# Optimization experiments

Measured on AMD Instinct MI355X. Metric: run time of the kernel, lower is better.

Reference implementation:

```python
import jax, jax.numpy as jnp
import numpy as np

N_ATOMS = 50000
N_EDGES = 600000
N_FEAT = 128      # n_atom_basis
N_FILT = 128      # n_filters
N_GAUSS = 32
N_CONV = 3
CUTOFF = 5.0
ATOMS_PER_MOL = 50
N_MOL = N_ATOMS // ATOMS_PER_MOL
N_KEYS = 2        # energy_0, energy_1
HIDDEN_RO = 64
LOG2 = float(np.log(2.0))


def ssp(x):
    # shifted softplus: softplus(x) - log(2)
    return jax.nn.softplus(x) - LOG2


def setup_inputs() -> dict:
    key = jax.random.key(0)
    ks = jax.random.split(key, 16)
    def w(k, shape, fan_in):
        return jax.random.normal(k, shape, dtype=jnp.float32) / np.sqrt(fan_in)
    return {
        "z": jax.random.randint(ks[0], (N_ATOMS,), 1, 100),
        "xyz": jax.random.normal(ks[1], (N_ATOMS, 3), dtype=jnp.float32) * 4.0,
        "nbr_list": jax.random.randint(ks[2], (N_EDGES, 2), 0, N_ATOMS),
        "mol_idx": jnp.arange(N_ATOMS, dtype=jnp.int32) // ATOMS_PER_MOL,
        "embed": jax.random.normal(ks[3], (100, N_FEAT), dtype=jnp.float32) * 0.1,
        "We1": w(ks[4], (N_CONV, N_GAUSS, N_FILT), N_GAUSS),
        "be1": jnp.zeros((N_CONV, N_FILT), jnp.float32),
        "We2": w(ks[5], (N_CONV, N_FILT, N_FILT), N_FILT),
        "be2": jnp.zeros((N_CONV, N_FILT), jnp.float32),
        "Wn": w(ks[6], (N_CONV, N_FEAT, N_FILT), N_FEAT),
        "bn": jnp.zeros((N_CONV, N_FILT), jnp.float32),
        "Wu1": w(ks[7], (N_CONV, N_FILT, N_FEAT), N_FILT),
        "bu1": jnp.zeros((N_CONV, N_FEAT), jnp.float32),
        "Wu2": w(ks[8], (N_CONV, N_FEAT, N_FEAT), N_FEAT),
        "bu2": jnp.zeros((N_CONV, N_FEAT), jnp.float32),
        "Wr1": w(ks[9], (N_KEYS, N_FEAT, HIDDEN_RO), N_FEAT),
        "br1": jnp.zeros((N_KEYS, HIDDEN_RO), jnp.float32),
        "Wr2": w(ks[10], (N_KEYS, HIDDEN_RO, 1), HIDDEN_RO),
        "br2": jnp.zeros((N_KEYS, 1), jnp.float32),
    }


def _forward(xyz, embed, We1, be1, We2, be2, Wn, bn, Wu1, bu1, Wu2, bu2,
             Wr1, br1, Wr2, br2, z, nbr_list, mol_idx):
    a0, a1 = nbr_list[:, 0], nbr_list[:, 1]
    # pairwise distances e = ||xyz_i - xyz_j||  -> [E,1]
    diff = xyz[a0] - xyz[a1]
    d = jnp.sqrt(jnp.sum(diff * diff, axis=1, keepdims=True))
    # Gaussian smearing on [0, cutoff]
    offs = jnp.linspace(0.0, CUTOFF, N_GAUSS).astype(xyz.dtype)
    width = offs[1] - offs[0]
    gauss = jnp.exp((-0.5 / (width * width)) * (d - offs[None, :]) ** 2)  # [E,G]
    r = embed[z]  # [N,F] atom embedding lookup
    for l in range(N_CONV):
        # edge filter MLP: G -> Filt -> Filt
        ef = ssp(gauss @ We1[l] + be1[l]) @ We2[l] + be2[l]       # [E,Filt]
        rf = r @ Wn[l] + bn[l]                                    # [N,Filt]
        m_ij = rf[a0] * ef                                        # gather * filter
        m_ji = rf[a1] * ef
        agg = (jax.ops.segment_sum(m_ij, a1, num_segments=N_ATOMS)
               + jax.ops.segment_sum(m_ji, a0, num_segments=N_ATOMS))
        # update MLP, residual add
        r = r + (ssp(agg @ Wu1[l] + bu1[l]) @ Wu2[l] + bu2[l])
    # per-key atomwise readout: F -> H -> 1
    h = ssp(jnp.einsum('nf,kfh->knh', r, Wr1) + br1[:, None, :])          # [K,N,H]
    e_atom = (jnp.einsum('knh,kho->kno', h, Wr2) + br2[:, None, :])[..., 0]  # [K,N]
    # sum atom energies per molecule (batch_and_sum)
    e_mol = jax.ops.segment_sum(e_atom.T, mol_idx, num_segments=N_MOL)    # [M,K]
    return e_mol


def reference(z, xyz, nbr_list, mol_idx, embed, We1, be1, We2, be2, Wn, bn,
              Wu1, bu1, Wu2, bu2, Wr1, br1, Wr2, br2):
    return _forward(xyz, embed, We1, be1, We2, be2, Wn, bn, Wu1, bu1,
                    Wu2, bu2, Wr1, br1, Wr2, br2, z, nbr_list, mol_idx)
```

## Files before the change

kernel.cpp:

```cpp
#include <hip/hip_runtime.h>
#include <math.h>

#define N_ATOMS   50000
#define N_PAD     50048
#define N_EDGES   600000
#define N_FEAT    128
#define N_GAUSS   32
#define N_CONV    3
#define N_MOLS    1000
#define HIDDEN_RO 64
#define CAP       64

#define TBL_N     1921
#define TBL_BPL   31
#define TBL_SCALE 256.0f
#define TBL_TMAX  1919.0f
#define NB_EDGE   2344
#define NB_BUILD  (N_CONV * TBL_BPL)
#define NB_EMBG   7
#define NB_WPREP  40

typedef unsigned int   uint32;
typedef unsigned short u16;
typedef __attribute__((ext_vector_type(8))) short bf16x8;
typedef __attribute__((ext_vector_type(4))) float f32x4;

__device__ __forceinline__ float ssp_f(float x) {
    float e = __expf(-fabsf(x));
    return fmaxf(x, 0.0f) + __logf(1.0f + e) - 0.6931471805599453f;
}
__device__ __forceinline__ uint32 f2bf_u(float x) {
    uint32 u = __float_as_uint(x);
    return (u + 0x7fffu + ((u >> 16) & 1u)) >> 16;
}
__device__ __forceinline__ uint32 pack2f(float a, float b) {
    return f2bf_u(a) | (f2bf_u(b) << 16);
}
__device__ __forceinline__ float bf_lo(uint32 u) { return __uint_as_float(u << 16); }
__device__ __forceinline__ float bf_hi(uint32 u) { return __uint_as_float(u & 0xffff0000u); }


#define FILL_START (NB_BUILD + NB_EMBG + NB_WPREP)
__global__ __launch_bounds__(256)
void k_uberA(const int* __restrict__ nbr, const float* __restrict__ xyz,
             int* __restrict__ cnt, uint32* __restrict__ inc32,
             const float* __restrict__ We1_all, const float* __restrict__ be1_all,
             const float* __restrict__ We2_all, const float* __restrict__ be2_all,
             uint32* __restrict__ tblI,
             const float* __restrict__ Wn, const float* __restrict__ bn,
             const float* __restrict__ Wu1,
             const float* __restrict__ Wu2, const float* __restrict__ Wr1,
             u16* __restrict__ Wt, const float* __restrict__ embed,
             float* __restrict__ Gp) {
    __shared__ float smemA[17408 / 4];
    int b = blockIdx.x;
    int t = threadIdx.x;

    if (b < NB_BUILD) {
        int l    = b / TBL_BPL;
        int row0 = (b % TBL_BPL) * 64;
        const float* We1 = We1_all + (size_t)l * N_GAUSS * N_FEAT;
        const float* be1 = be1_all + (size_t)l * N_FEAT;
        const float* We2 = We2_all + (size_t)l * N_FEAT * N_FEAT;
        const float* be2 = be2_all + (size_t)l * N_FEAT;
        uint32* tl = tblI + (size_t)l * TBL_N * 128;
        u16* h1T = (u16*)smemA;

        const float width = 5.0f / 31.0f;
        const float coef = -0.5f / (width * width);

        int tf = t & 15, te = t >> 4;
        int f0 = tf * 8, eb = te * 4;
        float dloc[4];
        #pragma unroll
        for (int i = 0; i < 4; ++i) dloc[i] = (float)(row0 + eb + i) * (1.0f / TBL_SCALE);

        float acc[4][8];
        #pragma unroll
        for (int i = 0; i < 4; ++i)
            #pragma unroll
            for (int j = 0; j < 8; ++j) acc[i][j] = 0.0f;

        for (int g = 0; g < N_GAUSS; ++g) {
            float mu = (float)g * width;
            float av[4];
            #pragma unroll
            for (int i = 0; i < 4; ++i) {
                float diff = dloc[i] - mu;
                av[i] = __expf(coef * diff * diff);
            }
            float4 w0 = *(const float4*)(We1 + g * N_FEAT + f0);
            float4 w1 = *(const float4*)(We1 + g * N_FEAT + f0 + 4);
            float wv[8] = {w0.x, w0.y, w0.z, w0.w, w1.x, w1.y, w1.z, w1.w};
            #pragma unroll
            for (int i = 0; i < 4; ++i)
                #pragma unroll
                for (int j = 0; j < 8; ++j) acc[i][j] += av[i] * wv[j];
        }
        #pragma unroll
        for (int j = 0; j < 8; ++j) {
            float bb2 = be1[f0 + j];
            uint2 hv;
            hv.x = pack2f(ssp_f(acc[0][j] + bb2), ssp_f(acc[1][j] + bb2));
            hv.y = pack2f(ssp_f(acc[2][j] + bb2), ssp_f(acc[3][j] + bb2));
            *(uint2*)&h1T[(f0 + j) * 68 + eb] = hv;
        }
        __syncthreads();

        #pragma unroll
        for (int i = 0; i < 4; ++i)
            #pragma unroll
            for (int j = 0; j < 8; ++j) acc[i][j] = 0.0f;
        #pragma unroll 2
        for (int c = 0; c < N_FEAT; ++c) {
            uint2 hv = *(const uint2*)&h1T[c * 68 + eb];
            float av[4] = {bf_lo(hv.x), bf_hi(hv.x), bf_lo(hv.y), bf_hi(hv.y)};
            float4 w0 = *(const float4*)(We2 + c * N_FEAT + f0);
            float4 w1 = *(const float4*)(We2 + c * N_FEAT + f0 + 4);
            float wv[8] = {w0.x, w0.y, w0.z, w0.w, w1.x, w1.y, w1.z, w1.w};
            #pragma unroll
            for (int i = 0; i < 4; ++i)
                #pragma unroll
                for (int j = 0; j < 8; ++j) acc[i][j] += av[i] * wv[j];
        }
        __syncthreads();

        uint32* pvS = (uint32*)smemA;
        #pragma unroll
        for (int i = 0; i < 4; ++i)
            #pragma unroll
            for (int p = 0; p < 4; ++p)
                pvS[(eb + i) * 65 + tf * 4 + p] =
                    pack2f(acc[i][2 * p]     + be2[f0 + 2 * p],
                           acc[i][2 * p + 1] + be2[f0 + 2 * p + 1]);
        __syncthreads();

        #pragma unroll
        for (int i = 0; i < 16; ++i) {
            int idx = t + 256 * i;
            int e = idx >> 6, fp = idx & 63;
            int ent = row0 + e;
            if (ent < TBL_N - 1) {
                if (e < 63) {
                    uint2 v2;
                    v2.x = pvS[e * 65 + fp];
                    v2.y = pvS[(e + 1) * 65 + fp];
                    *(uint2*)(tl + ((size_t)ent * 64 + fp) * 2) = v2;
                } else {
                    tl[((size_t)ent * 64 + fp) * 2] = pvS[63 * 65 + fp];
                }
            }
        }
        if (row0 > 0 && t < 64)
            tl[((size_t)(row0 - 1) * 64 + t) * 2 + 1] = pvS[t];
        return;
    }
    if (b < NB_BUILD + NB_EMBG) {
        int bb = b - NB_BUILD;
        int row = bb * 16 + (t >> 4);
        int tf = t & 15;
        if (row < 100) {
            float acc[8];
            #pragma unroll
            for (int j = 0; j < 8; ++j) acc[j] = 0.0f;
            for (int k = 0; k < N_FEAT; ++k) {
                float a = embed[row * N_FEAT + k];
                float4 w0 = *(const float4*)(Wn + k * N_FEAT + tf * 8);
                float4 w1 = *(const float4*)(Wn + k * N_FEAT + tf * 8 + 4);
                acc[0] += a * w0.x; acc[1] += a * w0.y;
                acc[2] += a * w0.z; acc[3] += a * w0.w;
                acc[4] += a * w1.x; acc[5] += a * w1.y;
                acc[6] += a * w1.z; acc[7] += a * w1.w;
            }
            #pragma unroll
            for (int j = 0; j < 8; ++j)
                Gp[row * N_FEAT + tf * 8 + j] = acc[j] + bn[tf * 8 + j];
        }
        return;
    }
    if (b < FILL_START) {
        int wb = b - NB_BUILD - NB_EMBG;
        int gid = wb * 256 + t;
        #pragma unroll
        for (int i = 0; i < 16; ++i) {
            int idx = gid + i * (NB_WPREP * 256);
            int j    = idx & 7;
            int lane = (idx >> 3) & 63;
            int cg   = (idx >> 9) & 7;
            int kc   = (idx >> 12) & 3;
            int mat  = idx >> 14;
            int col  = cg * 16 + (lane & 15);
            int k    = kc * 32 + (lane >> 4) * 8 + j;
            float v;
            if (mat < 3)      v = Wn [(size_t)mat * 16384 + k * 128 + col];
            else if (mat < 6) v = Wu1[(size_t)(mat - 3) * 16384 + k * 128 + col];
            else if (mat < 9) v = Wu2[(size_t)(mat - 6) * 16384 + k * 128 + col];
            else { int key = col >> 6, h = col & 63; v = Wr1[(size_t)key * 128 * 64 + k * 64 + h]; }
            Wt[(size_t)idx] = (u16)f2bf_u(v);
        }
        return;
    }
    {
        int cls = b & 7;
        int base = ((b - FILL_START) >> 3) * 2048;
        #pragma unroll
        for (int i = 0; i < 8; ++i) {
            int e = base + t + 256 * i;
            if (e < N_EDGES) {
                int a0 = nbr[2 * e], a1 = nbr[2 * e + 1];
                bool m0 = (a0 & 7) == cls, m1 = (a1 & 7) == cls;
                if (m0 | m1) {
                    float dx = xyz[3 * a0]     - xyz[3 * a1];
                    float dy = xyz[3 * a0 + 1] - xyz[3 * a1 + 1];
                    float dz = xyz[3 * a0 + 2] - xyz[3 * a1 + 2];
                    float d = sqrtf(dx * dx + dy * dy + dz * dz);
                    float tv = fminf(d * TBL_SCALE, TBL_TMAX);
                    uint32 tq = (uint32)(tv * 32.0f + 0.5f);
                    if (m1) {
                        int p1 = atomicAdd(&cnt[a1], 1);
                        if (p1 < CAP) inc32[((size_t)a1 << 6) | p1] = ((uint32)a0 << 16) | tq;
                    }
                    if (m0) {
                        int p0 = atomicAdd(&cnt[a0], 1);
                        if (p0 < CAP) inc32[((size_t)a0 << 6) | p0] = ((uint32)a1 << 16) | tq;
                    }
                }
            }
        }
    }
}

__global__ __launch_bounds__(256)
void k_gather(const int* __restrict__ z, const float* __restrict__ embed,
              const float* __restrict__ Gp, float* __restrict__ r,
              uint32* __restrict__ rf16) {
    int idx = blockIdx.x * 256 + threadIdx.x;
    if (idx >= N_PAD * 32) return;
    int n = idx >> 5, c4 = idx & 31;
    int zz = z[n < N_ATOMS ? n : 0];
    float4 v = *(const float4*)(embed + (size_t)zz * N_FEAT + c4 * 4);
    *(float4*)(r + (size_t)n * N_FEAT + c4 * 4) = v;
    float4 g = *(const float4*)(Gp + (size_t)zz * N_FEAT + c4 * 4);
    uint2 o;
    o.x = pack2f(g.x, g.y);
    o.y = pack2f(g.z, g.w);
    *(uint2*)(rf16 + (size_t)n * 64 + c4 * 2) = o;
}

__global__ __launch_bounds__(256)
void k_agg(const int* __restrict__ cnt, const uint32* __restrict__ inc32,
           const uint32* __restrict__ tblI, const uint32* __restrict__ rf,
           uint32* __restrict__ agg16) {
    int wv = threadIdx.x >> 6, lane = threadIdx.x & 63;
    int h = lane >> 5, lh = lane & 31;
    int n = blockIdx.x * 4 + wv;
    if (n >= N_ATOMS) return;
    int s = n << 6;
    int e = s + min(cnt[n], CAP);
    float a0 = 0.f, a1 = 0.f, a2 = 0.f, a3 = 0.f;
    int i = s;
    for (; i + 8 <= e; i += 8) {
        uint32 v[4];
        #pragma unroll
        for (int u = 0; u < 4; ++u) v[u] = inc32[i + 2 * u + h];
        int i0[4], oa[4];
        float fr[4];
        #pragma unroll
        for (int u = 0; u < 4; ++u) {
            oa[u] = v[u] >> 16;
            uint32 tq = v[u] & 0xffffu;
            i0[u] = tq >> 5;
            fr[u] = (float)(tq & 31u) * 0.03125f;
        }
        uint4 T[4];
        #pragma unroll
        for (int u = 0; u < 4; ++u) T[u] = *(const uint4*)(tblI + ((size_t)i0[u] * 64 + lh * 2) * 2);
        uint2 R[4];
        #pragma unroll
        for (int u = 0; u < 4; ++u) R[u] = *(const uint2*)(rf + (size_t)oa[u] * 64 + lh * 2);
        #pragma unroll
        for (int u = 0; u < 4; ++u) {
            float e0 = fmaf(fr[u], bf_lo(T[u].y) - bf_lo(T[u].x), bf_lo(T[u].x));
            float e1 = fmaf(fr[u], bf_hi(T[u].y) - bf_hi(T[u].x), bf_hi(T[u].x));
            float e2 = fmaf(fr[u], bf_lo(T[u].w) - bf_lo(T[u].z), bf_lo(T[u].z));
            float e3 = fmaf(fr[u], bf_hi(T[u].w) - bf_hi(T[u].z), bf_hi(T[u].z));
            a0 = fmaf(e0, bf_lo(R[u].x), a0);
            a1 = fmaf(e1, bf_hi(R[u].x), a1);
            a2 = fmaf(e2, bf_lo(R[u].y), a2);
            a3 = fmaf(e3, bf_hi(R[u].y), a3);
        }
    }
    for (; i < e; i += 2) {
        int idx = i + h;
        bool ok = idx < e;
        uint32 v = inc32[ok ? idx : s];
        int oa = v >> 16;
        uint32 tq = v & 0xffffu;
        int i0 = tq >> 5;
        float fr = (float)(tq & 31u) * 0.03125f;
        uint4 T = *(const uint4*)(tblI + ((size_t)i0 * 64 + lh * 2) * 2);
        uint2 R = *(const uint2*)(rf + (size_t)oa * 64 + lh * 2);
        float m = ok ? 1.0f : 0.0f;
        float e0 = fmaf(fr, bf_lo(T.y) - bf_lo(T.x), bf_lo(T.x));
        float e1 = fmaf(fr, bf_hi(T.y) - bf_hi(T.x), bf_hi(T.x));
        float e2 = fmaf(fr, bf_lo(T.w) - bf_lo(T.z), bf_lo(T.z));
        float e3 = fmaf(fr, bf_hi(T.w) - bf_hi(T.z), bf_hi(T.z));
        a0 = fmaf(e0, m * bf_lo(R.x), a0);
        a1 = fmaf(e1, m * bf_hi(R.x), a1);
        a2 = fmaf(e2, m * bf_lo(R.y), a2);
        a3 = fmaf(e3, m * bf_hi(R.y), a3);
    }
    a0 += __shfl_xor(a0, 32);
    a1 += __shfl_xor(a1, 32);
    a2 += __shfl_xor(a2, 32);
    a3 += __shfl_xor(a3, 32);
    if (h == 0) {
        uint2 o;
        o.x = pack2f(a0, a1);
        o.y = pack2f(a2, a3);
        *(uint2*)(agg16 + (size_t)n * 64 + lh * 2) = o;
    }
}

template <bool RO>
__global__ __launch_bounds__(256)
void k_update(const u16* __restrict__ agg16u,
              const float* __restrict__ bu1, const float* __restrict__ bu2,
              const u16* __restrict__ Wu1t, const u16* __restrict__ Wu2t,
              const u16* __restrict__ W3t, const float* __restrict__ b3,
              float* __restrict__ r, u16* __restrict__ rf16,
              const float* __restrict__ Wr2, const float* __restrict__ br2,
              const int* __restrict__ mol, float* __restrict__ out) {
    __shared__ u16 aT[32 * 136];
    __shared__ u16 hT[32 * 136];

    int tid = threadIdx.x;
    int w = tid >> 6, lane = tid & 63;
    int l15 = lane & 15, q = lane >> 4;
    int colbase = w * 32;
    size_t n0 = (size_t)blockIdx.x * 32;
    size_t fragoff = (size_t)(w * 2) * 512 + (size_t)lane * 8;

    bf16x8 bfr[4][2];
    #pragma unroll
    for (int kc = 0; kc < 4; ++kc)
        #pragma unroll
        for (int ntl = 0; ntl < 2; ++ntl)
            bfr[kc][ntl] = *(const bf16x8*)(Wu1t + kc * 4096 + ntl * 512 + fragoff);
    float rpre[2][2][4];
    #pragma unroll
    for (int ntl = 0; ntl < 2; ++ntl) {
        int col = colbase + ntl * 16 + l15;
        #pragma unroll
        for (int m = 0; m < 2; ++m)
            #pragma unroll
            for (int reg = 0; reg < 4; ++reg)
                rpre[ntl][m][reg] = r[(n0 + m * 16 + q * 4 + reg) * N_FEAT + col];
    }

    #pragma unroll
    for (int i = 0; i < 2; ++i) {
        int idx = tid + 256 * i;
        int row = idx >> 4, c = idx & 15;
        uint4 v = *(const uint4*)(agg16u + (n0 + row) * 128 + c * 8);
        *(uint4*)&aT[row * 136 + c * 8] = v;
    }
    __syncthreads();

    f32x4 acc[2][2];

    #pragma unroll
    for (int m = 0; m < 2; ++m)
        #pragma unroll
        for (int ntl = 0; ntl < 2; ++ntl) acc[m][ntl] = (f32x4){0.f, 0.f, 0.f, 0.f};
    #pragma unroll
    for (int kc = 0; kc < 4; ++kc)
        #pragma unroll
        for (int m = 0; m < 2; ++m) {
            bf16x8 a = *(const bf16x8*)(aT + (m * 16 + l15) * 136 + kc * 32 + q * 8);
            acc[m][0] = __builtin_amdgcn_mfma_f32_16x16x32_bf16(a, bfr[kc][0], acc[m][0], 0, 0, 0);
            acc[m][1] = __builtin_amdgcn_mfma_f32_16x16x32_bf16(a, bfr[kc][1], acc[m][1], 0, 0, 0);
        }
    #pragma unroll
    for (int ntl = 0; ntl < 2; ++ntl) {
        int col = colbase + ntl * 16 + l15;
        float bv = bu1[col];
        #pragma unroll
        for (int m = 0; m < 2; ++m)
            #pragma unroll
            for (int reg = 0; reg < 4; ++reg)
                hT[(m * 16 + q * 4 + reg) * 136 + col] = (u16)f2bf_u(ssp_f(acc[m][ntl][reg] + bv));
    }
    __syncthreads();

    #pragma unroll
    for (int kc = 0; kc < 4; ++kc)
        #pragma unroll
        for (int ntl = 0; ntl < 2; ++ntl)
            bfr[kc][ntl] = *(const bf16x8*)(Wu2t + kc * 4096 + ntl * 512 + fragoff);
    #pragma unroll
    for (int m = 0; m < 2; ++m)
        #pragma unroll
        for (int ntl = 0; ntl < 2; ++ntl) acc[m][ntl] = (f32x4){0.f, 0.f, 0.f, 0.f};
    #pragma unroll
    for (int kc = 0; kc < 4; ++kc)
        #pragma unroll
        for (int m = 0; m < 2; ++m) {
            bf16x8 a = *(const bf16x8*)(hT + (m * 16 + l15) * 136 + kc * 32 + q * 8);
            acc[m][0] = __builtin_amdgcn_mfma_f32_16x16x32_bf16(a, bfr[kc][0], acc[m][0], 0, 0, 0);
            acc[m][1] = __builtin_amdgcn_mfma_f32_16x16x32_bf16(a, bfr[kc][1], acc[m][1], 0, 0, 0);
        }
    __syncthreads();
    #pragma unroll
    for (int ntl = 0; ntl < 2; ++ntl) {
        int col = colbase + ntl * 16 + l15;
        float bv = bu2[col];
        #pragma unroll
        for (int m = 0; m < 2; ++m)
            #pragma unroll
            for (int reg = 0; reg < 4; ++reg) {
                int row = m * 16 + q * 4 + reg;
                float v = acc[m][ntl][reg] + bv + rpre[ntl][m][reg];
                if (!RO) r[(n0 + row) * N_FEAT + col] = v;
                aT[row * 136 + col] = (u16)f2bf_u(v);
            }
    }
    __syncthreads();

    #pragma unroll
    for (int kc = 0; kc < 4; ++kc)
        #pragma unroll
        for (int ntl = 0; ntl < 2; ++ntl)
            bfr[kc][ntl] = *(const bf16x8*)(W3t + kc * 4096 + ntl * 512 + fragoff);
    #pragma unroll
    for (int m = 0; m < 2; ++m)
        #pragma unroll
        for (int ntl = 0; ntl < 2; ++ntl) acc[m][ntl] = (f32x4){0.f, 0.f, 0.f, 0.f};
    #pragma unroll
    for (int kc = 0; kc < 4; ++kc)
        #pragma unroll
        for (int m = 0; m < 2; ++m) {
            bf16x8 a = *(const bf16x8*)(aT + (m * 16 + l15) * 136 + kc * 32 + q * 8);
            acc[m][0] = __builtin_amdgcn_mfma_f32_16x16x32_bf16(a, bfr[kc][0], acc[m][0], 0, 0, 0);
            acc[m][1] = __builtin_amdgcn_mfma_f32_16x16x32_bf16(a, bfr[kc][1], acc[m][1], 0, 0, 0);
        }

    if (!RO) {
        #pragma unroll
        for (int ntl = 0; ntl < 2; ++ntl) {
            int col = colbase + ntl * 16 + l15;
            float bv = b3[col];
            #pragma unroll
            for (int m = 0; m < 2; ++m)
                #pragma unroll
                for (int reg = 0; reg < 4; ++reg) {
                    int row = m * 16 + q * 4 + reg;
                    rf16[(n0 + row) * N_FEAT + col] = (u16)f2bf_u(acc[m][ntl][reg] + bv);
                }
        }
    } else {
        float (*red)[4][17] = (float(*)[4][17])aT;
        __syncthreads();
        float b1v[2], w2v[2];
        #pragma unroll
        for (int ntl = 0; ntl < 2; ++ntl) {
            int col = colbase + ntl * 16 + l15;
            b1v[ntl] = b3[col];
            w2v[ntl] = Wr2[col];
        }
        #pragma unroll
        for (int m = 0; m < 2; ++m)
            #pragma unroll
            for (int reg = 0; reg < 4; ++reg) {
                float pk = ssp_f(acc[m][0][reg] + b1v[0]) * w2v[0]
                         + ssp_f(acc[m][1][reg] + b1v[1]) * w2v[1];
                red[m * 16 + q * 4 + reg][w][l15] = pk;
            }
        __syncthreads();
        if (tid < 64) {
            int row = tid & 31, key = tid >> 5;
            int atom = (int)n0 + row;
            if (atom < N_ATOMS) {
                float s = br2[key];
                #pragma unroll
                for (int j = 0; j < 16; ++j)
                    s += red[row][2 * key][j] + red[row][2 * key + 1][j];
                atomicAdd(&out[mol[atom] * 2 + key], s);
            }
        }
    }
}

extern "C" void kernel_launch(void* const* d_in, const int* in_sizes, int n_in,
                              void* d_out, int out_size, void* d_ws, size_t ws_size,
                              hipStream_t stream) {
    const int*   z     = (const int*)d_in[0];
    const float* xyz   = (const float*)d_in[1];
    const int*   nbr   = (const int*)d_in[2];
    const int*   mol   = (const int*)d_in[3];
    const float* embed = (const float*)d_in[4];
    const float* We1   = (const float*)d_in[5];
    const float* be1   = (const float*)d_in[6];
    const float* We2   = (const float*)d_in[7];
    const float* be2   = (const float*)d_in[8];
    const float* Wn    = (const float*)d_in[9];
    const float* bn    = (const float*)d_in[10];
    const float* Wu1   = (const float*)d_in[11];
    const float* bu1   = (const float*)d_in[12];
    const float* Wu2   = (const float*)d_in[13];
    const float* bu2   = (const float*)d_in[14];
    const float* Wr1   = (const float*)d_in[15];
    const float* br1   = (const float*)d_in[16];
    const float* Wr2   = (const float*)d_in[17];
    const float* br2   = (const float*)d_in[18];
    float* out = (float*)d_out;

    float* ws = (float*)d_ws;
    const size_t NRP = (size_t)N_PAD * N_FEAT;
    const size_t NHP = (size_t)N_PAD * 64;
    float*  r_buf  = ws;
    uint32* agg16  = (uint32*)(ws + NRP);
    uint32* rf16   = agg16 + NHP;
    int*    cnt    = (int*)(rf16 + NHP);
    uint32* inc32  = (uint32*)(cnt + 50048);
    uint32* tblI   = inc32 + (size_t)N_ATOMS * CAP;
    u16*    Wt     = (u16*)(tblI + (size_t)3 * TBL_N * 128);
    float*  Gp     = (float*)(Wt + 10 * 16384);

    hipMemsetAsync(d_out, 0, (size_t)out_size * sizeof(float), stream);
    hipMemsetAsync(cnt, 0, 50000 * sizeof(int), stream);

    k_uberA<<<FILL_START + NB_EDGE, 256, 0, stream>>>(
        nbr, xyz, cnt, inc32, We1, be1, We2, be2, tblI,
        Wn, bn, Wu1, Wu2, Wr1, Wt, embed, Gp);

    k_gather<<<(N_PAD * 32) / 256, 256, 0, stream>>>(z, embed, Gp, r_buf, rf16);

    const int GA2 = N_PAD / 32;
    for (int l = 0; l < N_CONV; ++l) {
        k_agg<<<(N_ATOMS + 3) / 4, 256, 0, stream>>>(cnt, inc32,
                                                     tblI + (size_t)l * TBL_N * 128,
                                                     rf16, agg16);
        const u16* Wu1t = Wt + (size_t)(3 + l) * 16384;
        const u16* Wu2t = Wt + (size_t)(6 + l) * 16384;
        if (l < N_CONV - 1) {
            k_update<false><<<GA2, 256, 0, stream>>>((const u16*)agg16, bu1 + l * 128,
                                                     bu2 + l * 128, Wu1t, Wu2t,
                                                     Wt + (size_t)(l + 1) * 16384,
                                                     bn + (l + 1) * 128,
                                                     r_buf, (u16*)rf16, Wr2, br2, mol, out);
        } else {
            k_update<true><<<GA2, 256, 0, stream>>>((const u16*)agg16, bu1 + l * 128,
                                                    bu2 + l * 128, Wu1t, Wu2t,
                                                    Wt + (size_t)9 * 16384, br1,
                                                    r_buf, (u16*)rf16, Wr2, br2, mol, out);
        }
    }
}
```

Baseline: 412.3 us.

## Merge memsets and embed GEMV into pre-kernel, fold gather into uber kernel

Replaces the two hipMemsetAsync calls with a small pre-kernel that also computes the embedding-times-Wn table, then folds the atom gather into the big uber kernel. Edge-fill blocks now come first so the long edge scatter starts early. In k_agg, each wave loads its 64 incidence entries once and broadcasts them with shuffles instead of reloading per step. The aim is fewer launches and less redundant global loading, at the cost of one extra dependency stage for the precomputed table.

Result: no change. 406.4 us, median of 3 (-1.4%).

```diff
diff --git a/kernel.cpp b/kernel.cpp
--- a/kernel.cpp
+++ b/kernel.cpp
@@ -17,8 +17,11 @@
 #define TBL_TMAX  1919.0f
 #define NB_EDGE   2344
 #define NB_BUILD  (N_CONV * TBL_BPL)
-#define NB_EMBG   7
 #define NB_WPREP  40
+#define NB_GATH   6256
+#define BUILD_START NB_EDGE
+#define WPREP_START (NB_EDGE + NB_BUILD)
+#define GATH_START  (NB_EDGE + NB_BUILD + NB_WPREP)
 
 typedef unsigned int   uint32;
 typedef unsigned short u16;
@@ -39,125 +42,13 @@
 __device__ __forceinline__ float bf_lo(uint32 u) { return __uint_as_float(u << 16); }
 __device__ __forceinline__ float bf_hi(uint32 u) { return __uint_as_float(u & 0xffff0000u); }
 
-
-#define FILL_START (NB_BUILD + NB_EMBG + NB_WPREP)
 __global__ __launch_bounds__(256)
-void k_uberA(const int* __restrict__ nbr, const float* __restrict__ xyz,
-             int* __restrict__ cnt, uint32* __restrict__ inc32,
-             const float* __restrict__ We1_all, const float* __restrict__ be1_all,
-             const float* __restrict__ We2_all, const float* __restrict__ be2_all,
-             uint32* __restrict__ tblI,
-             const float* __restrict__ Wn, const float* __restrict__ bn,
-             const float* __restrict__ Wu1,
-             const float* __restrict__ Wu2, const float* __restrict__ Wr1,
-             u16* __restrict__ Wt, const float* __restrict__ embed,
-             float* __restrict__ Gp) {
-    __shared__ float smemA[17408 / 4];
-    int b = blockIdx.x;
-    int t = threadIdx.x;
-
-    if (b < NB_BUILD) {
-        int l    = b / TBL_BPL;
-        int row0 = (b % TBL_BPL) * 64;
-        const float* We1 = We1_all + (size_t)l * N_GAUSS * N_FEAT;
-        const float* be1 = be1_all + (size_t)l * N_FEAT;
-        const float* We2 = We2_all + (size_t)l * N_FEAT * N_FEAT;
-        const float* be2 = be2_all + (size_t)l * N_FEAT;
-        uint32* tl = tblI + (size_t)l * TBL_N * 128;
-        u16* h1T = (u16*)smemA;
-
-        const float width = 5.0f / 31.0f;
-        const float coef = -0.5f / (width * width);
-
-        int tf = t & 15, te = t >> 4;
-        int f0 = tf * 8, eb = te * 4;
-        float dloc[4];
-        #pragma unroll
-        for (int i = 0; i < 4; ++i) dloc[i] = (float)(row0 + eb + i) * (1.0f / TBL_SCALE);
-
-        float acc[4][8];
-        #pragma unroll
-        for (int i = 0; i < 4; ++i)
-            #pragma unroll
-            for (int j = 0; j < 8; ++j) acc[i][j] = 0.0f;
-
-        for (int g = 0; g < N_GAUSS; ++g) {
-            float mu = (float)g * width;
-            float av[4];
-            #pragma unroll
-            for (int i = 0; i < 4; ++i) {
-                float diff = dloc[i] - mu;
-                av[i] = __expf(coef * diff * diff);
-            }
-            float4 w0 = *(const float4*)(We1 + g * N_FEAT + f0);
-            float4 w1 = *(const float4*)(We1 + g * N_FEAT + f0 + 4);
-            float wv[8] = {w0.x, w0.y, w0.z, w0.w, w1.x, w1.y, w1.z, w1.w};
-            #pragma unroll
-            for (int i = 0; i < 4; ++i)
-                #pragma unroll
-                for (int j = 0; j < 8; ++j) acc[i][j] += av[i] * wv[j];
-        }
-        #pragma unroll
-        for (int j = 0; j < 8; ++j) {
-            float bb2 = be1[f0 + j];
-            uint2 hv;
-            hv.x = pack2f(ssp_f(acc[0][j] + bb2), ssp_f(acc[1][j] + bb2));
-            hv.y = pack2f(ssp_f(acc[2][j] + bb2), ssp_f(acc[3][j] + bb2));
-            *(uint2*)&h1T[(f0 + j) * 68 + eb] = hv;
-        }
-        __syncthreads();
-
-        #pragma unroll
-        for (int i = 0; i < 4; ++i)
-            #pragma unroll
-            for (int j = 0; j < 8; ++j) acc[i][j] = 0.0f;
-        #pragma unroll 2
-        for (int c = 0; c < N_FEAT; ++c) {
-            uint2 hv = *(const uint2*)&h1T[c * 68 + eb];
-            float av[4] = {bf_lo(hv.x), bf_hi(hv.x), bf_lo(hv.y), bf_hi(hv.y)};
-            float4 w0 = *(const float4*)(We2 + c * N_FEAT + f0);
-            float4 w1 = *(const float4*)(We2 + c * N_FEAT + f0 + 4);
-            float wv[8] = {w0.x, w0.y, w0.z, w0.w, w1.x, w1.y, w1.z, w1.w};
-            #pragma unroll
-            for (int i = 0; i < 4; ++i)
-                #pragma unroll
-                for (int j = 0; j < 8; ++j) acc[i][j] += av[i] * wv[j];
-        }
-        __syncthreads();
-
-        uint32* pvS = (uint32*)smemA;
-        #pragma unroll
-        for (int i = 0; i < 4; ++i)
-            #pragma unroll
-            for (int p = 0; p < 4; ++p)
-                pvS[(eb + i) * 65 + tf * 4 + p] =
-                    pack2f(acc[i][2 * p]     + be2[f0 + 2 * p],
-                           acc[i][2 * p + 1] + be2[f0 + 2 * p + 1]);
-        __syncthreads();
-
-        #pragma unroll
-        for (int i = 0; i < 16; ++i) {
-            int idx = t + 256 * i;
-            int e = idx >> 6, fp = idx & 63;
-            int ent = row0 + e;
-            if (ent < TBL_N - 1) {
-                if (e < 63) {
-                    uint2 v2;
-                    v2.x = pvS[e * 65 + fp];
-                    v2.y = pvS[(e + 1) * 65 + fp];
-                    *(uint2*)(tl + ((size_t)ent * 64 + fp) * 2) = v2;
-                } else {
-                    tl[((size_t)ent * 64 + fp) * 2] = pvS[63 * 65 + fp];
-                }
-            }
-        }
-        if (row0 > 0 && t < 64)
-            tl[((size_t)(row0 - 1) * 64 + t) * 2 + 1] = pvS[t];
-        return;
-    }
-    if (b < NB_BUILD + NB_EMBG) {
-        int bb = b - NB_BUILD;
-        int row = bb * 16 + (t >> 4);
+void k_pre(const float* __restrict__ embed, const float* __restrict__ Wn,
+           const float* __restrict__ bn, float* __restrict__ Gp,
+           int* __restrict__ cnt, float* __restrict__ out, int out_size) {
+    int b = blockIdx.x, t = threadIdx.x;
+    if (b < 7) {
+        int row = b * 16 + (t >> 4);
         int tf = t & 15;
         if (row < 100) {
             float acc[8];
@@ -176,33 +67,34 @@
             for (int j = 0; j < 8; ++j)
                 Gp[row * N_FEAT + tf * 8 + j] = acc[j] + bn[tf * 8 + j];
         }
-        return;
-    }
-    if (b < FILL_START) {
-        int wb = b - NB_BUILD - NB_EMBG;
-        int gid = wb * 256 + t;
-        #pragma unroll
-        for (int i = 0; i < 16; ++i) {
-            int idx = gid + i * (NB_WPREP * 256);
-            int j    = idx & 7;
-            int lane = (idx >> 3) & 63;
-            int cg   = (idx >> 9) & 7;
-            int kc   = (idx >> 12) & 3;
-            int mat  = idx >> 14;
-            int col  = cg * 16 + (lane & 15);
-            int k    = kc * 32 + (lane >> 4) * 8 + j;
-            float v;
-            if (mat < 3)      v = Wn [(size_t)mat * 16384 + k * 128 + col];
-            else if (mat < 6) v = Wu1[(size_t)(mat - 3) * 16384 + k * 128 + col];
-            else if (mat < 9) v = Wu2[(size_t)(mat - 6) * 16384 + k * 128 + col];
-            else { int key = col >> 6, h = col & 63; v = Wr1[(size_t)key * 128 * 64 + k * 64 + h]; }
-            Wt[(size_t)idx] = (u16)f2bf_u(v);
-        }
-        return;
-    }
-    {
+    } else if (b < 56) {
+        int i = (b - 7) * 1024 + t * 4;
+        if (i < 50048) *(int4*)(cnt + i) = make_int4(0, 0, 0, 0);
+    } else {
+        for (int j = t; j < out_size; j += 256) out[j] = 0.0f;
+    }
+}
+
+__global__ __launch_bounds__(256)
+void k_uberA(const int* __restrict__ nbr, const float* __restrict__ xyz,
+             int* __restrict__ cnt, uint32* __restrict__ inc32,
+             const float* __restrict__ We1_all, const float* __restrict__ be1_all,
+             const float* __restrict__ We2_all, const float* __restrict__ be2_all,
+             uint32* __restrict__ tblI,
+             const float* __restrict__ Wn,
+             const float* __restrict__ Wu1,
+             const float* __restrict__ Wu2, const float* __restrict__ Wr1,
+             u16* __restrict__ Wt,
+             const int* __restrict__ z, const float* __restrict__ embed,
+             const float* __restrict__ Gp, float* __restrict__ r,
+             uint32* __restrict__ rf16) {
+    __shared__ float smemA[17408 / 4];
+    int b = blockIdx.x;
+    int t = threadIdx.x;
+
+    if (b < NB_EDGE) {
         int cls = b & 7;
-        int base = ((b - FILL_START) >> 3) * 2048;
+        int base = (b >> 3) * 2048;
         #pragma unroll
         for (int i = 0; i < 8; ++i) {
             int e = base + t + 256 * i;
@@ -227,24 +119,142 @@
                 }
             }
         }
-    }
-}
-
-__global__ __launch_bounds__(256)
-void k_gather(const int* __restrict__ z, const float* __restrict__ embed,
-              const float* __restrict__ Gp, float* __restrict__ r,
-              uint32* __restrict__ rf16) {
-    int idx = blockIdx.x * 256 + threadIdx.x;
-    if (idx >= N_PAD * 32) return;
-    int n = idx >> 5, c4 = idx & 31;
-    int zz = z[n < N_ATOMS ? n : 0];
-    float4 v = *(const float4*)(embed + (size_t)zz * N_FEAT + c4 * 4);
-    *(float4*)(r + (size_t)n * N_FEAT + c4 * 4) = v;
-    float4 g = *(const float4*)(Gp + (size_t)zz * N_FEAT + c4 * 4);
-    uint2 o;
-    o.x = pack2f(g.x, g.y);
-    o.y = pack2f(g.z, g.w);
-    *(uint2*)(rf16 + (size_t)n * 64 + c4 * 2) = o;
+        return;
+    }
+    if (b < WPREP_START) {
+        int bb   = b - BUILD_START;
+        int l    = bb / TBL_BPL;
+        int row0 = (bb % TBL_BPL) * 64;
+        const float* We1 = We1_all + (size_t)l * N_GAUSS * N_FEAT;
+        const float* be1 = be1_all + (size_t)l * N_FEAT;
+        const float* We2 = We2_all + (size_t)l * N_FEAT * N_FEAT;
+        const float* be2 = be2_all + (size_t)l * N_FEAT;
+        uint32* tl = tblI + (size_t)l * TBL_N * 128;
+        u16* h1T = (u16*)smemA;
+
+        const float width = 5.0f / 31.0f;
+        const float coef = -0.5f / (width * width);
+
+        int tf = t & 15, te = t >> 4;
+        int f0 = tf * 8, eb = te * 4;
+        float dloc[4];
+        #pragma unroll
+        for (int i = 0; i < 4; ++i) dloc[i] = (float)(row0 + eb + i) * (1.0f / TBL_SCALE);
+
+        float acc[4][8];
+        #pragma unroll
+        for (int i = 0; i < 4; ++i)
+            #pragma unroll
+            for (int j = 0; j < 8; ++j) acc[i][j] = 0.0f;
+
+        for (int g = 0; g < N_GAUSS; ++g) {
+            float mu = (float)g * width;
+            float av[4];
+            #pragma unroll
+            for (int i = 0; i < 4; ++i) {
+                float diff = dloc[i] - mu;
+                av[i] = __expf(coef * diff * diff);
+            }
+            float4 w0 = *(const float4*)(We1 + g * N_FEAT + f0);
+            float4 w1 = *(const float4*)(We1 + g * N_FEAT + f0 + 4);
+            float wv[8] = {w0.x, w0.y, w0.z, w0.w, w1.x, w1.y, w1.z, w1.w};
+            #pragma unroll
+            for (int i = 0; i < 4; ++i)
+                #pragma unroll
+                for (int j = 0; j < 8; ++j) acc[i][j] += av[i] * wv[j];
+        }
+        #pragma unroll
+        for (int j = 0; j < 8; ++j) {
+            float bb2 = be1[f0 + j];
+            uint2 hv;
+            hv.x = pack2f(ssp_f(acc[0][j] + bb2), ssp_f(acc[1][j] + bb2));
+            hv.y = pack2f(ssp_f(acc[2][j] + bb2), ssp_f(acc[3][j] + bb2));
+            *(uint2*)&h1T[(f0 + j) * 68 + eb] = hv;
+        }
+        __syncthreads();
+
+        #pragma unroll
+        for (int i = 0; i < 4; ++i)
+            #pragma unroll
+            for (int j = 0; j < 8; ++j) acc[i][j] = 0.0f;
+        #pragma unroll 2
+        for (int c = 0; c < N_FEAT; ++c) {
+            uint2 hv = *(const uint2*)&h1T[c * 68 + eb];
+            float av[4] = {bf_lo(hv.x), bf_hi(hv.x), bf_lo(hv.y), bf_hi(hv.y)};
+            float4 w0 = *(const float4*)(We2 + c * N_FEAT + f0);
+            float4 w1 = *(const float4*)(We2 + c * N_FEAT + f0 + 4);
+            float wv[8] = {w0.x, w0.y, w0.z, w0.w, w1.x, w1.y, w1.z, w1.w};
+            #pragma unroll
+            for (int i = 0; i < 4; ++i)
+                #pragma unroll
+                for (int j = 0; j < 8; ++j) acc[i][j] += av[i] * wv[j];
+        }
+        __syncthreads();
+
+        uint32* pvS = (uint32*)smemA;
+        #pragma unroll
+        for (int i = 0; i < 4; ++i)
+            #pragma unroll
+            for (int p = 0; p < 4; ++p)
+                pvS[(eb + i) * 65 + tf * 4 + p] =
+                    pack2f(acc[i][2 * p]     + be2[f0 + 2 * p],
+                           acc[i][2 * p + 1] + be2[f0 + 2 * p + 1]);
+        __syncthreads();
+
+        #pragma unroll
+        for (int i = 0; i < 16; ++i) {
+            int idx = t + 256 * i;
+            int e = idx >> 6, fp = idx & 63;
+            int ent = row0 + e;
+            if (ent < TBL_N - 1) {
+                if (e < 63) {
+                    uint2 v2;
+                    v2.x = pvS[e * 65 + fp];
+                    v2.y = pvS[(e + 1) * 65 + fp];
+                    *(uint2*)(tl + ((size_t)ent * 64 + fp) * 2) = v2;
+                } else {
+                    tl[((size_t)ent * 64 + fp) * 2] = pvS[63 * 65 + fp];
+                }
+            }
+        }
+        if (row0 > 0 && t < 64)
+            tl[((size_t)(row0 - 1) * 64 + t) * 2 + 1] = pvS[t];
+        return;
+    }
+    if (b < GATH_START) {
+        int wb = b - WPREP_START;
+        int gid = wb * 256 + t;
+        #pragma unroll
+        for (int i = 0; i < 16; ++i) {
+            int idx = gid + i * (NB_WPREP * 256);
+            int j    = idx & 7;
+            int lane = (idx >> 3) & 63;
+            int cg   = (idx >> 9) & 7;
+            int kc   = (idx >> 12) & 3;
+            int mat  = idx >> 14;
+            int col  = cg * 16 + (lane & 15);
+            int k    = kc * 32 + (lane >> 4) * 8 + j;
+            float v;
+            if (mat < 3)      v = Wn [(size_t)mat * 16384 + k * 128 + col];
+            else if (mat < 6) v = Wu1[(size_t)(mat - 3) * 16384 + k * 128 + col];
+            else if (mat < 9) v = Wu2[(size_t)(mat - 6) * 16384 + k * 128 + col];
+            else { int key = col >> 6, h = col & 63; v = Wr1[(size_t)key * 128 * 64 + k * 64 + h]; }
+            Wt[(size_t)idx] = (u16)f2bf_u(v);
+        }
+        return;
+    }
+    {
+        int idx = (b - GATH_START) * 256 + t;
+        int n = idx >> 5, c4 = idx & 31;
+        int zz = z[n < N_ATOMS ? n : 0];
+        float4 v = *(const float4*)(embed + (size_t)zz * N_FEAT + c4 * 4);
+        *(float4*)(r + (size_t)n * N_FEAT + c4 * 4) = v;
+        float4 g = *(const float4*)(Gp + (size_t)zz * N_FEAT + c4 * 4);
+        uint2 o;
+        o.x = pack2f(g.x, g.y);
+        o.y = pack2f(g.z, g.w);
+        *(uint2*)(rf16 + (size_t)n * 64 + c4 * 2) = o;
+    }
 }
 
 __global__ __launch_bounds__(256)
@@ -256,13 +266,14 @@
     int n = blockIdx.x * 4 + wv;
     if (n >= N_ATOMS) return;
     int s = n << 6;
-    int e = s + min(cnt[n], CAP);
+    int c = min(cnt[n], CAP);
+    uint32 vAll = inc32[s + lane];
     float a0 = 0.f, a1 = 0.f, a2 = 0.f, a3 = 0.f;
-    int i = s;
-    for (; i + 8 <= e; i += 8) {
+    int i = 0;
+    for (; i + 8 <= c; i += 8) {
         uint32 v[4];
         #pragma unroll
-        for (int u = 0; u < 4; ++u) v[u] = inc32[i + 2 * u + h];
+        for (int u = 0; u < 4; ++u) v[u] = __shfl(vAll, i + 2 * u + h);
         int i0[4], oa[4];
         float fr[4];
         #pragma unroll
@@ -290,10 +301,10 @@
             a3 = fmaf(e3, bf_hi(R[u].y), a3);
         }
     }
-    for (; i < e; i += 2) {
-        int idx = i + h;
-        bool ok = idx < e;
-        uint32 v = inc32[ok ? idx : s];
+    for (; i < c; i += 2) {
+        int src = i + h;
+        bool ok = src < c;
+        uint32 v = __shfl(vAll, ok ? src : 0);
         int oa = v >> 16;
         uint32 tq = v & 0xffffu;
         int i0 = tq >> 5;
@@ -527,14 +538,11 @@
     u16*    Wt     = (u16*)(tblI + (size_t)3 * TBL_N * 128);
     float*  Gp     = (float*)(Wt + 10 * 16384);
 
-    hipMemsetAsync(d_out, 0, (size_t)out_size * sizeof(float), stream);
-    hipMemsetAsync(cnt, 0, 50000 * sizeof(int), stream);
-
-    k_uberA<<<FILL_START + NB_EDGE, 256, 0, stream>>>(
+    k_pre<<<57, 256, 0, stream>>>(embed, Wn, bn, Gp, cnt, out, out_size);
+
+    k_uberA<<<GATH_START + NB_GATH, 256, 0, stream>>>(
         nbr, xyz, cnt, inc32, We1, be1, We2, be2, tblI,
-        Wn, bn, Wu1, Wu2, Wr1, Wt, embed, Gp);
-
-    k_gather<<<(N_PAD * 32) / 256, 256, 0, stream>>>(z, embed, Gp, r_buf, rf16);
+        Wn, Wu1, Wu2, Wr1, Wt, z, embed, Gp, r_buf, rf16);
 
     const int GA2 = N_PAD / 32;
     for (int l = 0; l < N_CONV; ++l) {
```
